# Kernel tuning notes

Measured on AMD Instinct MI355X. Metric: run time of the kernel, lower is better.

## Reference

```python
import jax, jax.numpy as jnp
import numpy as np

IN_FEATURES = 2048
OUT_FEATURES = 2048
BATCH = 4096


def setup_inputs() -> dict:
    key = jax.random.key(0)
    k1, k2, k3, k4 = jax.random.split(key, 4)
    bound = 1.0 / (IN_FEATURES ** 0.5)
    x_re = jax.random.normal(k1, (BATCH, IN_FEATURES), dtype=jnp.float32)
    x_im = jax.random.normal(k2, (BATCH, IN_FEATURES), dtype=jnp.float32)
    # filters: (out_features, in_features), re/im each uniform(-bound, bound)
    w_re = jax.random.uniform(k3, (OUT_FEATURES, IN_FEATURES), dtype=jnp.float32, minval=-bound, maxval=bound)
    w_im = jax.random.uniform(k4, (OUT_FEATURES, IN_FEATURES), dtype=jnp.float32, minval=-bound, maxval=bound)
    return {"x_re": x_re, "x_im": x_im, "w_re": w_re, "w_im": w_im}


def reference(x_re, x_im, w_re, w_im):
    # Complex linear: (x_re + i x_im) @ (w_re + i w_im)^T, expressed as 4 real GEMMs.
    # Equivalent to torch: (inputs.unsqueeze(1) * filters).sum(-1) with complex64.
    out_re = jnp.einsum('bi,oi->bo', x_re, w_re) - jnp.einsum('bi,oi->bo', x_im, w_im)
    out_im = jnp.einsum('bi,oi->bo', x_re, w_im) + jnp.einsum('bi,oi->bo', x_im, w_re)
    # stack re/im -> (2, batch, out) to keep a single real-dtype output
    return jnp.stack([out_re, out_im], axis=0)
```

## Files before the change

kernel.cpp:

```cpp
#include <hip/hip_runtime.h>

typedef __bf16 bf16_t;
typedef __bf16 bf16x8 __attribute__((ext_vector_type(8)));
typedef __bf16 bf16x4 __attribute__((ext_vector_type(4)));
typedef float f32x4 __attribute__((ext_vector_type(4)));

#define M_DIM 4096
#define N_DIM 4096
#define K_DIM 4096
#define OUTF 2048
#define INF 2048
#define LDK 4096
#define NT 64

__global__ __launch_bounds__(256) void pack_ab(
    const float* __restrict__ xre, const float* __restrict__ xim,
    const float* __restrict__ wre, const float* __restrict__ wim,
    bf16_t* __restrict__ Abf, bf16_t* __restrict__ Bbf)
{
  size_t gid = (size_t)blockIdx.x * 256 + threadIdx.x;
  size_t e8  = gid * 8;
  const size_t MAT = (size_t)4096 * 4096;
  bool isB = e8 >= MAT;
  size_t e = isB ? (e8 - MAT) : e8;
  int row = (int)(e >> 12);
  int k   = (int)(e & 4095);

  const float* src;
  float s = 1.0f;
  if (!isB) {
    src = (k < INF) ? (xre + (size_t)row * INF + k)
                    : (xim + (size_t)row * INF + (k - INF));
  } else {
    if (row < OUTF) {
      if (k < INF) { src = wre + (size_t)row * INF + k; }
      else         { src = wim + (size_t)row * INF + (k - INF); s = -1.0f; }
    } else {
      int o = row - OUTF;
      src = (k < INF) ? (wim + (size_t)o * INF + k)
                      : (wre + (size_t)o * INF + (k - INF));
    }
  }
  const float4* p = reinterpret_cast<const float4*>(src);
  float4 f0 = p[0];
  float4 f1 = p[1];
  bf16x8 v;
  v[0] = (bf16_t)(f0.x * s); v[1] = (bf16_t)(f0.y * s);
  v[2] = (bf16_t)(f0.z * s); v[3] = (bf16_t)(f0.w * s);
  v[4] = (bf16_t)(f1.x * s); v[5] = (bf16_t)(f1.y * s);
  v[6] = (bf16_t)(f1.z * s); v[7] = (bf16_t)(f1.w * s);
  bf16_t* dst = (isB ? Bbf : Abf) + e;
  *reinterpret_cast<bf16x8*>(dst) = v;
}

__device__ __forceinline__ void gld_lds16(const void* g, void* l) {
  __builtin_amdgcn_global_load_lds(
      (const __attribute__((address_space(1))) void*)g,
      (__attribute__((address_space(3))) void*)l,
      16, 0, 0);
}


template<int QM, int QN>
__device__ __forceinline__ void mfma_quad(f32x4 (&acc)[8][4],
                                          const bf16x8 (&aF)[4][2],
                                          const bf16x8 (&bF)[2][2]) {
  __builtin_amdgcn_s_setprio(1);
#pragma unroll
  for (int m = 0; m < 4; ++m)
#pragma unroll
    for (int n = 0; n < 2; ++n) {
      f32x4 v = acc[QM * 4 + m][QN * 2 + n];
      v = __builtin_amdgcn_mfma_f32_16x16x32_bf16(aF[m][0], bF[n][0], v, 0, 0, 0);
      v = __builtin_amdgcn_mfma_f32_16x16x32_bf16(aF[m][1], bF[n][1], v, 0, 0, 0);
      acc[QM * 4 + m][QN * 2 + n] = v;
    }
  __builtin_amdgcn_s_setprio(0);
}

__global__ __launch_bounds__(512, 2) void gemm256(
    const bf16_t* __restrict__ A, const bf16_t* __restrict__ B,
    float* __restrict__ out)
{
  __shared__ alignas(16) bf16_t lds[2 * 32768];
  char* Lb = (char*)lds;

  const int tid  = threadIdx.x;
  const int lane = tid & 63;
  const int wid  = tid >> 6;
  const int wm   = wid >> 2;
  const int wn   = wid & 3;
  const int lr   = lane & 15;
  const int kg   = (lane >> 4) * 16;
  const int xm   = ((lr & 3) << 4) | (((lr >> 2) & 1) << 6);

  int bid = blockIdx.x;
  int swz = (bid & 7) * 32 + (bid >> 3);
  const int bm = swz >> 4;
  const int bn = swz & 15;

  int rS[2], kS[2];
#pragma unroll
  for (int j = 0; j < 2; ++j) {
    int P   = j * 8192 + tid * 16;
    int row = P >> 7;
    int p   = P & 127;
    int L   = p ^ ((row & 3) << 4) ^ (((row >> 2) & 1) << 6);
    rS[j] = row;
    kS[j] = L >> 1;
  }
  const bf16_t* As0 = A + (size_t)(bm * 256 + rS[0]) * LDK + kS[0];
  const bf16_t* As1 = A + (size_t)(bm * 256 + rS[1]) * LDK + kS[1];
  const bf16_t* Bs0 = B + (size_t)(bn * 256 + rS[0]) * LDK + kS[0];
  const bf16_t* Bs1 = B + (size_t)(bn * 256 + rS[1]) * LDK + kS[1];
  const int dst16 = tid * 16;

#define STAGE_A(t, h, c) do {                                                  \
    gld_lds16(As0 + (size_t)(h) * 128 * LDK + (t) * 64,                        \
              Lb + (c) * 65536 + (h) * 16384 + dst16);                         \
    gld_lds16(As1 + (size_t)(h) * 128 * LDK + (t) * 64,                        \
              Lb + (c) * 65536 + (h) * 16384 + 8192 + dst16);                  \
  } while (0)
#define STAGE_B(t, h, c) do {                                                  \
    gld_lds16(Bs0 + (size_t)(h) * 128 * LDK + (t) * 64,                        \
              Lb + (c) * 65536 + 32768 + (h) * 16384 + dst16);                 \
    gld_lds16(Bs1 + (size_t)(h) * 128 * LDK + (t) * 64,                        \
              Lb + (c) * 65536 + 32768 + (h) * 16384 + 8192 + dst16);          \
  } while (0)
#define RD_A(c, qm, m, ks)                                                     \
  (*(const bf16x8*)(Lb + (c) * 65536 + wm * 16384 +                            \
                    ((qm) * 64 + (m) * 16 + lr) * 128 +                        \
                    ((((ks) * 64) | kg) ^ xm)))
#define RD_B(c, qn, n, ks)                                                     \
  (*(const bf16x8*)(Lb + (c) * 65536 + 32768 + (wn >> 1) * 16384 +             \
                    ((wn & 1) * 64 + (qn) * 32 + (n) * 16 + lr) * 128 +        \
                    ((((ks) * 64) | kg) ^ xm)))
#define BAR()    __builtin_amdgcn_s_barrier()
#define LGKM0()  asm volatile("s_waitcnt lgkmcnt(0)" ::: "memory")

  f32x4 acc[8][4];
#pragma unroll
  for (int i = 0; i < 8; ++i)
#pragma unroll
    for (int j = 0; j < 4; ++j)
      acc[i][j] = (f32x4){0.f, 0.f, 0.f, 0.f};

  STAGE_A(0, 0, 0); STAGE_A(0, 1, 0);
  STAGE_B(0, 0, 0); STAGE_B(0, 1, 0);
  STAGE_A(1, 0, 1); STAGE_A(1, 1, 1);
  STAGE_B(1, 0, 1); STAGE_B(1, 1, 1);
  asm volatile("s_waitcnt vmcnt(8)" ::: "memory");
  BAR();

  for (int t = 0; t < NT; ++t) {
    const int c = t & 1;
    bf16x8 aF[4][2], bF0[2][2], bF1[2][2];

#pragma unroll
    for (int m = 0; m < 4; ++m) {
      aF[m][0] = RD_A(c, 0, m, 0);
      aF[m][1] = RD_A(c, 0, m, 1);
    }
#pragma unroll
    for (int n = 0; n < 2; ++n) {
      bF0[n][0] = RD_B(c, 0, n, 0);
      bF0[n][1] = RD_B(c, 0, n, 1);
    }
    BAR(); LGKM0();
    mfma_quad<0, 0>(acc, aF, bF0);
    BAR();

#pragma unroll
    for (int n = 0; n < 2; ++n) {
      bF1[n][0] = RD_B(c, 1, n, 0);
      bF1[n][1] = RD_B(c, 1, n, 1);
    }
    BAR(); LGKM0();
    mfma_quad<0, 1>(acc, aF, bF1);
    BAR();

#pragma unroll
    for (int m = 0; m < 4; ++m) {
      aF[m][0] = RD_A(c, 1, m, 0);
      aF[m][1] = RD_A(c, 1, m, 1);
    }
    if (t + 2 < NT) { STAGE_B(t + 2, 0, c); STAGE_B(t + 2, 1, c); }
    BAR(); LGKM0();
    mfma_quad<1, 1>(acc, aF, bF1);
    BAR();

    if (t + 2 < NT) { STAGE_A(t + 2, 0, c); STAGE_A(t + 2, 1, c); }
    mfma_quad<1, 0>(acc, aF, bF0);
    if (t + 2 < NT) {
      asm volatile("s_waitcnt vmcnt(8)" ::: "memory");
    } else if (t + 1 < NT) {
      asm volatile("s_waitcnt vmcnt(0)" ::: "memory");
    }
    BAR();
  }

  const size_t imOff = (size_t)M_DIM * OUTF;
  const int fq = (lane >> 4) * 4;
  const bool isIm = (bn * 256) >= OUTF;
  float* obase = out + (isIm ? imOff : 0);
  const int colBase = bn * 256 - (isIm ? OUTF : 0) + wn * 64;
#pragma unroll
  for (int ar = 0; ar < 8; ++ar) {
    int gr = bm * 256 + wm * 128 + ar * 16 + fq;
#pragma unroll
    for (int cc = 0; cc < 4; ++cc) {
      int gc = colBase + cc * 16 + lr;
#pragma unroll
      for (int j = 0; j < 4; ++j)
        obase[(size_t)(gr + j) * OUTF + gc] = acc[ar][cc][j];
    }
  }
#undef STAGE_A
#undef STAGE_B
#undef RD_A
#undef RD_B
#undef BAR
#undef LGKM0
}

__global__ __launch_bounds__(256) void gemm_fused(
    const float* __restrict__ xre, const float* __restrict__ xim,
    const float* __restrict__ wre, const float* __restrict__ wim,
    float* __restrict__ out)
{
  __shared__ alignas(16) bf16_t As[128 * 40];
  __shared__ alignas(16) bf16_t Bs[128 * 40];

  int tid = threadIdx.x;
  int bid = blockIdx.x;
  int swz = (bid & 7) * 128 + (bid >> 3);
  int bm = swz >> 5;
  int bn = swz & 31;

  int lane = tid & 63;
  int w    = tid >> 6;
  int wm   = (w >> 1) * 64;
  int wn   = (w & 1) * 64;
  int lr   = lane & 15;
  int lk   = (lane >> 4) * 8;

  f32x4 acc[4][4];
#pragma unroll
  for (int m = 0; m < 4; ++m)
#pragma unroll
    for (int n = 0; n < 4; ++n)
      acc[m][n] = (f32x4){0.f, 0.f, 0.f, 0.f};

  int srow = tid >> 3;
  int scol = (tid & 7) * 4;

  bool nIm  = (bn * 128) >= OUTF;
  int nbase = nIm ? (bn * 128 - OUTF) : (bn * 128);

  for (int kt = 0; kt < K_DIM / 32; ++kt) {
    int k0 = kt * 32;
    bool kHi = (k0 >= INF);
    int kk = kHi ? (k0 - INF) : k0;

    const float* Asrc = (kHi ? xim : xre) + (size_t)(bm * 128) * INF + kk;
    const float* Bsrc;
    float s = 1.0f;
    if (!nIm) { if (!kHi) { Bsrc = wre; } else { Bsrc = wim; s = -1.0f; } }
    else      { Bsrc = kHi ? wre : wim; }
    Bsrc += (size_t)nbase * INF + kk;

    float4 av[4], bv[4];
#pragma unroll
    for (int i = 0; i < 4; ++i) {
      av[i] = *reinterpret_cast<const float4*>(Asrc + (size_t)(srow + i * 32) * INF + scol);
      bv[i] = *reinterpret_cast<const float4*>(Bsrc + (size_t)(srow + i * 32) * INF + scol);
    }
    __syncthreads();
#pragma unroll
    for (int i = 0; i < 4; ++i) {
      bf16x4 a4, b4;
      a4[0] = (bf16_t)av[i].x; a4[1] = (bf16_t)av[i].y;
      a4[2] = (bf16_t)av[i].z; a4[3] = (bf16_t)av[i].w;
      b4[0] = (bf16_t)(bv[i].x * s); b4[1] = (bf16_t)(bv[i].y * s);
      b4[2] = (bf16_t)(bv[i].z * s); b4[3] = (bf16_t)(bv[i].w * s);
      *reinterpret_cast<bf16x4*>(&As[(srow + i * 32) * 40 + scol]) = a4;
      *reinterpret_cast<bf16x4*>(&Bs[(srow + i * 32) * 40 + scol]) = b4;
    }
    __syncthreads();

    bf16x8 a[4], b[4];
#pragma unroll
    for (int m = 0; m < 4; ++m)
      a[m] = *reinterpret_cast<const bf16x8*>(&As[(wm + m * 16 + lr) * 40 + lk]);
#pragma unroll
    for (int n = 0; n < 4; ++n)
      b[n] = *reinterpret_cast<const bf16x8*>(&Bs[(wn + n * 16 + lr) * 40 + lk]);
#pragma unroll
    for (int m = 0; m < 4; ++m)
#pragma unroll
      for (int n = 0; n < 4; ++n)
        acc[m][n] = __builtin_amdgcn_mfma_f32_16x16x32_bf16(a[m], b[n], acc[m][n], 0, 0, 0);
  }
  __syncthreads();

  const size_t imOff = (size_t)M_DIM * OUTF;
  int fq = (lane >> 4) * 4;
#pragma unroll
  for (int m = 0; m < 4; ++m) {
    int gr = bm * 128 + wm + m * 16 + fq;
#pragma unroll
    for (int n = 0; n < 4; ++n) {
      int gc = bn * 128 + wn + n * 16 + lr;
      float* dst = (gc < OUTF) ? (out + (size_t)gr * OUTF + gc)
                               : (out + imOff + (size_t)gr * OUTF + (gc - OUTF));
#pragma unroll
      for (int j = 0; j < 4; ++j)
        dst[(size_t)j * OUTF] = acc[m][n][j];
    }
  }
}

extern "C" void kernel_launch(void* const* d_in, const int* in_sizes, int n_in,
                              void* d_out, int out_size, void* d_ws, size_t ws_size,
                              hipStream_t stream) {
  const float* xre = (const float*)d_in[0];
  const float* xim = (const float*)d_in[1];
  const float* wre = (const float*)d_in[2];
  const float* wim = (const float*)d_in[3];
  float* out = (float*)d_out;

  const size_t need = (size_t)2 * 4096 * 4096 * sizeof(bf16_t);
  if (ws_size >= need) {
    bf16_t* Abf = (bf16_t*)d_ws;
    bf16_t* Bbf = Abf + (size_t)4096 * 4096;
    hipLaunchKernelGGL(pack_ab, dim3(16384), dim3(256), 0, stream,
                       xre, xim, wre, wim, Abf, Bbf);
    hipLaunchKernelGGL(gemm256, dim3(256), dim3(512), 0, stream,
                       Abf, Bbf, out);
  } else {
    hipLaunchKernelGGL(gemm_fused, dim3(1024), dim3(256), 0, stream,
                       xre, xim, wre, wim, out);
  }
}
```

Before: 143.5 us.

## Issue all LDS fragment reads up front and use partial lgkmcnt waits

The main loop used to read A/B fragments from LDS in four phases, each separated by barriers and full lgkmcnt(0) waits. It now issues all fragment reads for the tile at the start, pinning their order with sched_barrier. Counted lgkmcnt waits let the first MFMA quads start while later reads are still in flight. Only one barrier is kept before the next tile's global-to-LDS staging. The cost is more live fragment registers, which risks register pressure or lower occupancy, and it depends on the fixed LDS read issue order for the counts to be correct.

```diff
diff --git a/kernel.cpp b/kernel.cpp
--- a/kernel.cpp
+++ b/kernel.cpp
@@ -135,8 +135,8 @@
   (*(const bf16x8*)(Lb + (c) * 65536 + 32768 + (wn >> 1) * 16384 +             \
                     ((wn & 1) * 64 + (qn) * 32 + (n) * 16 + lr) * 128 +        \
                     ((((ks) * 64) | kg) ^ xm)))
-#define BAR()    __builtin_amdgcn_s_barrier()
-#define LGKM0()  asm volatile("s_waitcnt lgkmcnt(0)" ::: "memory")
+#define BAR()   __builtin_amdgcn_s_barrier()
+#define SB()    __builtin_amdgcn_sched_barrier(0)
 
   f32x4 acc[8][4];
 #pragma unroll
@@ -154,43 +154,52 @@
 
   for (int t = 0; t < NT; ++t) {
     const int c = t & 1;
-    bf16x8 aF[4][2], bF0[2][2], bF1[2][2];
+    bf16x8 a0[4][2], a1[4][2], b0[2][2], b1[2][2];
 
 #pragma unroll
     for (int m = 0; m < 4; ++m) {
-      aF[m][0] = RD_A(c, 0, m, 0);
-      aF[m][1] = RD_A(c, 0, m, 1);
+      a0[m][0] = RD_A(c, 0, m, 0);
+      a0[m][1] = RD_A(c, 0, m, 1);
     }
 #pragma unroll
     for (int n = 0; n < 2; ++n) {
-      bF0[n][0] = RD_B(c, 0, n, 0);
-      bF0[n][1] = RD_B(c, 0, n, 1);
-    }
-    BAR(); LGKM0();
-    mfma_quad<0, 0>(acc, aF, bF0);
+      b0[n][0] = RD_B(c, 0, n, 0);
+      b0[n][1] = RD_B(c, 0, n, 1);
+    }
+    SB();
+#pragma unroll
+    for (int n = 0; n < 2; ++n) {
+      b1[n][0] = RD_B(c, 1, n, 0);
+      b1[n][1] = RD_B(c, 1, n, 1);
+    }
+    SB();
+#pragma unroll
+    for (int m = 0; m < 4; ++m) {
+      a1[m][0] = RD_A(c, 1, m, 0);
+      a1[m][1] = RD_A(c, 1, m, 1);
+    }
+    SB();
+
+    asm volatile("s_waitcnt lgkmcnt(12)" ::: "memory");
+    SB();
+    mfma_quad<0, 0>(acc, a0, b0);
+
+    asm volatile("s_waitcnt lgkmcnt(8)" ::: "memory");
+    SB();
+    mfma_quad<0, 1>(acc, a0, b1);
+
+    asm volatile("s_waitcnt lgkmcnt(0)" ::: "memory");
+    SB();
     BAR();
 
-#pragma unroll
-    for (int n = 0; n < 2; ++n) {
-      bF1[n][0] = RD_B(c, 1, n, 0);
-      bF1[n][1] = RD_B(c, 1, n, 1);
-    }
-    BAR(); LGKM0();
-    mfma_quad<0, 1>(acc, aF, bF1);
-    BAR();
-
-#pragma unroll
-    for (int m = 0; m < 4; ++m) {
-      aF[m][0] = RD_A(c, 1, m, 0);
-      aF[m][1] = RD_A(c, 1, m, 1);
-    }
-    if (t + 2 < NT) { STAGE_B(t + 2, 0, c); STAGE_B(t + 2, 1, c); }
-    BAR(); LGKM0();
-    mfma_quad<1, 1>(acc, aF, bF1);
-    BAR();
-
-    if (t + 2 < NT) { STAGE_A(t + 2, 0, c); STAGE_A(t + 2, 1, c); }
-    mfma_quad<1, 0>(acc, aF, bF0);
+    if (t + 2 < NT) {
+      STAGE_B(t + 2, 0, c); STAGE_B(t + 2, 1, c);
+      STAGE_A(t + 2, 0, c); STAGE_A(t + 2, 1, c);
+    }
+    SB();
+    mfma_quad<1, 1>(acc, a1, b1);
+    mfma_quad<1, 0>(acc, a1, b0);
+
     if (t + 2 < NT) {
       asm volatile("s_waitcnt vmcnt(8)" ::: "memory");
     } else if (t + 1 < NT) {
@@ -220,7 +229,7 @@
 #undef RD_A
 #undef RD_B
 #undef BAR
-#undef LGKM0
+#undef SB
 }
 
 __global__ __launch_bounds__(256) void gemm_fused(
```

After: 145.1 us. Within noise of the previous version (+1.1%).
